# Performance work log

Measured on AMD Instinct MI355X. Metric: run time of the kernel, lower is better.

## Reference

```python
import jax, jax.numpy as jnp
import numpy as np

EPS = 1e-5

def batchnorm2d(x, gamma, beta):
    # training-mode BN over (N, T, V) per channel; x: [N, C, T, V]
    mean = jnp.mean(x, axis=(0, 2, 3), keepdims=True)
    var = jnp.var(x, axis=(0, 2, 3), keepdims=True)
    xhat = (x - mean) * jax.lax.rsqrt(var + EPS)
    return xhat * gamma[None, :, None, None] + beta[None, :, None, None]

def temporal_shift(x, theta, stride):
    # learnable per-channel temporal shift with linear interpolation, zero pad
    # x: [N, C, T, V], theta: [C]
    N, C, T, V = x.shape
    T_out = T // stride
    t = jnp.arange(T_out, dtype=theta.dtype)
    pos = t[None, :] * stride + theta[:, None]          # [C, T_out]
    i0 = jnp.floor(pos).astype(jnp.int32)
    frac = (pos - i0.astype(theta.dtype))[None, :, :, None]  # [1,C,T_out,1]
    cidx = jnp.arange(C)[:, None]                        # [C, 1]

    def gather(idx):
        valid = (idx >= 0) & (idx < T)
        g = x[:, cidx, jnp.clip(idx, 0, T - 1), :]       # [N, C, T_out, V]
        return jnp.where(valid[None, :, :, None], g, 0.0)

    return gather(i0) * (1.0 - frac) + gather(i0 + 1) * frac

def setup_inputs() -> dict:
    key = jax.random.key(0)
    k = jax.random.split(key, 6)
    N, Cin, Cout, T, V = 64, 256, 256, 64, 25
    x = jax.random.normal(k[0], (N, Cin, T, V), dtype=jnp.float32)
    # kaiming normal fan_out for 1x1 conv: std = sqrt(2 / (Cout*1*1))
    conv_w = jax.random.normal(k[1], (Cout, Cin), dtype=jnp.float32) * np.float32(np.sqrt(2.0 / Cout))
    conv_b = jnp.zeros((Cout,), dtype=jnp.float32)
    bn1_g = jnp.ones((Cin,), dtype=jnp.float32)
    bn1_b = jnp.zeros((Cin,), dtype=jnp.float32)
    bn2_g = jnp.ones((Cin,), dtype=jnp.float32)   # bn_init(bn2, 1)
    bn2_b = jnp.zeros((Cin,), dtype=jnp.float32)
    theta_in = jax.random.uniform(k[2], (Cin,), jnp.float32, -1.0, 1.0)
    theta_out = jax.random.uniform(k[3], (Cout,), jnp.float32, -1.0, 1.0)
    return {"x": x, "conv_w": conv_w, "conv_b": conv_b,
            "bn1_g": bn1_g, "bn1_b": bn1_b, "bn2_g": bn2_g, "bn2_b": bn2_b,
            "theta_in": theta_in, "theta_out": theta_out}

def reference(x, conv_w, conv_b, bn1_g, bn1_b, bn2_g, bn2_b, theta_in, theta_out):
    stride = 1
    h = batchnorm2d(x, bn1_g, bn1_b)
    h = temporal_shift(h, theta_in, 1)
    h = jnp.einsum('nctv,oc->notv', h, conv_w) + conv_b[None, :, None, None]
    h = jax.nn.relu(h)
    h = temporal_shift(h, theta_out, stride)
    h = batchnorm2d(h, bn2_g, bn2_b)
    return h
```

## Files before the change

kernel.cpp:

```cpp
#include <hip/hip_runtime.h>


#define EPSV 1e-5f
constexpr int Nn = 64, Cc = 256, Tt = 64, Vv = 25;
constexpr int TV = Tt * Vv;
constexpr int CTV = Cc * TV;
constexpr float Minv = 1.0f / (Nn * TV);

typedef short short8 __attribute__((ext_vector_type(8)));
typedef float floatx4 __attribute__((ext_vector_type(4)));

__device__ __forceinline__ unsigned short f2bf(float f) {
    unsigned int u = __builtin_bit_cast(unsigned int, f);
    u += 0x7FFFu + ((u >> 16) & 1u);
    return (unsigned short)(u >> 16);
}
__device__ __forceinline__ float bf2f(unsigned short h) {
    unsigned int u = ((unsigned int)h) << 16;
    return __builtin_bit_cast(float, u);
}
__device__ __forceinline__ float bflo(unsigned int w) {
    return __builtin_bit_cast(float, w << 16);
}
__device__ __forceinline__ float bfhi(unsigned int w) {
    return __builtin_bit_cast(float, w & 0xFFFF0000u);
}
__device__ __forceinline__ void unp8v(uint4 u, float* o) {
    o[0] = bflo(u.x); o[1] = bfhi(u.x); o[2] = bflo(u.y); o[3] = bfhi(u.y);
    o[4] = bflo(u.z); o[5] = bfhi(u.z); o[6] = bflo(u.w); o[7] = bfhi(u.w);
}
__device__ __forceinline__ void gload_lds16(const void* g, void* l) {
    __builtin_amdgcn_global_load_lds((const __attribute__((address_space(1))) void*)g,
                                     (__attribute__((address_space(3))) void*)l, 16, 0, 0);
}

__global__ __launch_bounds__(256) void k_stats_shift(const float* __restrict__ x,
                                                     const float* __restrict__ theta,
                                                     float* __restrict__ sacc,
                                                     float* __restrict__ qacc,
                                                     unsigned short* __restrict__ ht) {
    int c0 = blockIdx.x * 64;
    int E0 = blockIdx.y * 200;
    int n  = blockIdx.z;
    int tid = threadIdx.x;
    __shared__ __attribute__((aligned(16))) unsigned short xt[256][68];
    __shared__ int   pd[64];
    __shared__ float pf[64];
    if (tid < 64) {
        float th = theta[c0 + tid];
        float fd = floorf(th);
        pd[tid] = (int)fd;
        pf[tid] = th - fd;
    }
    int lo = E0 - 28; if (lo < 0) lo = 0;
    int hi = E0 + 228; if (hi > 1600) hi = 1600;
    int ldsoff = lo - (E0 - 28);
    int nf4 = (hi - lo) >> 2;
    {
        int cp = tid >> 3, li = tid & 7;
        int ca = 2 * cp;
        const float4* xr0 = (const float4*)(x + (size_t)n * CTV + (size_t)(c0 + ca) * TV + lo);
        const float4* xr1 = (const float4*)(x + (size_t)n * CTV + (size_t)(c0 + ca + 1) * TV + lo);
        float s0 = 0.f, q0 = 0.f, s1 = 0.f, q1 = 0.f;
        for (int i = li; i < nf4; i += 8) {
            float4 v0 = xr0[i], v1 = xr1[i];
            int r = ldsoff + i * 4;
#pragma unroll
            for (int k = 0; k < 4; ++k) {
                float a = ((const float*)&v0)[k];
                float b = ((const float*)&v1)[k];
                bool in = (unsigned)(r + k - 28) < 200u;
                if (in) { s0 += a; q0 += a * a; s1 += b; q1 += b * b; }
                unsigned int pk = (unsigned int)f2bf(a) | (((unsigned int)f2bf(b)) << 16);
                *(unsigned int*)&xt[r + k][ca] = pk;
            }
        }
        for (int off = 4; off; off >>= 1) {
            s0 += __shfl_down(s0, off); q0 += __shfl_down(q0, off);
            s1 += __shfl_down(s1, off); q1 += __shfl_down(q1, off);
        }
        if (li == 0) {
            atomicAdd(&sacc[c0 + ca], s0);     atomicAdd(&qacc[c0 + ca], q0);
            atomicAdd(&sacc[c0 + ca + 1], s1); atomicAdd(&qacc[c0 + ca + 1], q1);
        }
    }
    __syncthreads();
    int cseg = tid & 7, er = tid >> 3;
    int cb = cseg * 8;
    int dk[8]; float fk[8];
#pragma unroll
    for (int k = 0; k < 8; ++k) { dk[k] = pd[cb + k]; fk[k] = pf[cb + k]; }
    for (int it = 0; it < 7; ++it) {
        int tv_l = er + it * 32;
        if (tv_l >= 200) break;
        int e = E0 + tv_l;
        float A8[8], B8[8], C8[8];
        {
            const unsigned short* rA = &xt[tv_l + 3][cb];
            const unsigned short* rB = &xt[tv_l + 28][cb];
            const unsigned short* rC = &xt[tv_l + 53][cb];
            uint2 a0 = *(const uint2*)rA, a1 = *(const uint2*)(rA + 4);
            uint2 b0 = *(const uint2*)rB, b1 = *(const uint2*)(rB + 4);
            uint2 g0 = *(const uint2*)rC, g1 = *(const uint2*)(rC + 4);
            A8[0]=bflo(a0.x); A8[1]=bfhi(a0.x); A8[2]=bflo(a0.y); A8[3]=bfhi(a0.y);
            A8[4]=bflo(a1.x); A8[5]=bfhi(a1.x); A8[6]=bflo(a1.y); A8[7]=bfhi(a1.y);
            B8[0]=bflo(b0.x); B8[1]=bfhi(b0.x); B8[2]=bflo(b0.y); B8[3]=bfhi(b0.y);
            B8[4]=bflo(b1.x); B8[5]=bfhi(b1.x); B8[6]=bflo(b1.y); B8[7]=bfhi(b1.y);
            C8[0]=bflo(g0.x); C8[1]=bfhi(g0.x); C8[2]=bflo(g0.y); C8[3]=bfhi(g0.y);
            C8[4]=bflo(g1.x); C8[5]=bfhi(g1.x); C8[6]=bflo(g1.y); C8[7]=bfhi(g1.y);
        }
        unsigned int w4[4];
#pragma unroll
        for (int k = 0; k < 8; ++k) {
            int d = dk[k]; float f = fk[k];
            float x0 = (d < 0) ? A8[k] : B8[k];
            float x1 = (d < 0) ? B8[k] : C8[k];
            int e0 = e + 25 * d;
            float v0 = ((unsigned)e0 < 1600u) ? x0 : 0.f;
            float v1 = ((unsigned)(e0 + 25) < 1600u) ? x1 : 0.f;
            unsigned short hb = f2bf(v0 + f * (v1 - v0));
            if (k & 1) w4[k >> 1] |= ((unsigned int)hb) << 16;
            else       w4[k >> 1] = hb;
        }
        uint4 st = { w4[0], w4[1], w4[2], w4[3] };
        *(uint4*)(ht + (size_t)(n * 1600 + e) * 256 + c0 + cb) = st;
    }
}

__global__ __launch_bounds__(256) void k_params(const float* __restrict__ w,
                                                const float* __restrict__ bias,
                                                const float* __restrict__ sacc,
                                                const float* __restrict__ qacc,
                                                const float* __restrict__ g,
                                                const float* __restrict__ b,
                                                const float* __restrict__ theta,
                                                unsigned short* __restrict__ wb,
                                                float* __restrict__ b2all,
                                                float* __restrict__ s0v,
                                                float* __restrict__ s63v) {
    int o = blockIdx.x, c = threadIdx.x;
    float mean = sacc[c] * Minv;
    float var  = qacc[c] * Minv - mean * mean;
    float sc = g[c] * rsqrtf(var + EPSV);
    float tc = b[c] - mean * sc;
    float th = theta[c];
    float fd = floorf(th);
    int d = (int)fd;
    float f = th - fd;
    float wv = w[o * 256 + c];
    wb[o * 256 + c] = f2bf(wv * sc);
    float wtc = wv * tc;
    float r0  = (d < 0) ? wtc * (1.f - f) : 0.f;
    float r63 = (d == 0) ? wtc * f : 0.f;
    for (int off = 32; off; off >>= 1) {
        wtc += __shfl_down(wtc, off);
        r0  += __shfl_down(r0, off);
        r63 += __shfl_down(r63, off);
    }
    __shared__ float aux[3][4];
    if ((c & 63) == 0) { int wi = c >> 6; aux[0][wi] = wtc; aux[1][wi] = r0; aux[2][wi] = r63; }
    __syncthreads();
    if (c == 0) {
        b2all[o] = bias[o] + aux[0][0] + aux[0][1] + aux[0][2] + aux[0][3];
        s0v[o]  = aux[1][0] + aux[1][1] + aux[1][2] + aux[1][3];
        s63v[o] = aux[2][0] + aux[2][1] + aux[2][2] + aux[2][3];
    }
}

__global__ __launch_bounds__(256, 2) void k_gemm(const unsigned short* __restrict__ ht,
                                                 const unsigned short* __restrict__ wb,
                                                 const float* __restrict__ b2all,
                                                 const float* __restrict__ s0v,
                                                 const float* __restrict__ s63v,
                                                 unsigned short* __restrict__ y) {
    int j0 = blockIdx.x * 128;
    int tid = threadIdx.x;
    int w = tid >> 6, lane = tid & 63;
    int quad = lane >> 4, l16 = lane & 15;
    __shared__ __attribute__((aligned(16))) unsigned short smem[256 * 136];
    unsigned short* A = smem;
    unsigned short* B = smem + 256 * 32;
    floatx4 acc[4][8] = {};
    int srowA = w * 64 + (lane >> 2);
    int srowB = w * 32 + (lane >> 2);
    int skc = (lane & 3) * 8;
    const unsigned short* wp = wb + (size_t)srowA * 256 + skc;
    const unsigned short* hp = ht + (size_t)(j0 + srowB) * 256 + skc;
    for (int k0 = 0; k0 < 256; k0 += 32) {
        __syncthreads();
#pragma unroll
        for (int a = 0; a < 4; ++a)
            gload_lds16(wp + (size_t)a * 16 * 256 + k0, A + (w * 64 + a * 16) * 32);
#pragma unroll
        for (int a = 0; a < 2; ++a)
            gload_lds16(hp + (size_t)a * 16 * 256 + k0, B + (w * 32 + a * 16) * 32);
        __syncthreads();
        short8 af[4], bf[8];
#pragma unroll
        for (int m = 0; m < 4; ++m)
            af[m] = *(const short8*)&A[(w * 64 + m * 16 + l16) * 32 + quad * 8];
#pragma unroll
        for (int jt = 0; jt < 8; ++jt)
            bf[jt] = *(const short8*)&B[(jt * 16 + l16) * 32 + quad * 8];
#pragma unroll
        for (int m = 0; m < 4; ++m)
#pragma unroll
            for (int jt = 0; jt < 8; ++jt)
                acc[m][jt] = __builtin_amdgcn_mfma_f32_16x16x32_bf16(af[m], bf[jt], acc[m][jt], 0, 0, 0);
    }
    __syncthreads();
    unsigned short* Cl = smem;
#pragma unroll
    for (int m = 0; m < 4; ++m) {
        int ob = w * 64 + m * 16 + quad * 4;
#pragma unroll
        for (int r = 0; r < 4; ++r) {
            int o = ob + r;
            float bb = b2all[o], e0 = s0v[o], e63 = s63v[o];
#pragma unroll
            for (int jt = 0; jt < 8; ++jt) {
                int jj = j0 + jt * 16;
                int nn = jj / 1600;
                int tvb = jj - nn * 1600 + l16;
                float bia = bb - (tvb < 25 ? e0 : 0.f) - (tvb >= 1575 ? e63 : 0.f);
                float v = acc[m][jt][r] + bia;
                v = v > 0.f ? v : 0.f;
                Cl[o * 136 + jt * 16 + l16] = f2bf(v);
            }
        }
    }
    __syncthreads();
    int li = tid & 15, orow = tid >> 4;
#pragma unroll
    for (int pass = 0; pass < 16; ++pass) {
        int o = orow + pass * 16;
        uint4 vv = *(const uint4*)&Cl[o * 136 + li * 8];
        int j = j0 + li * 8;
        int nn = j / 1600;
        int tv = j - nn * 1600;
        *(uint4*)(y + (size_t)nn * CTV + (size_t)o * TV + tv) = vv;
    }
}

__global__ __launch_bounds__(256) void k_bn2_stats(const unsigned short* __restrict__ y,
                                                   float* __restrict__ acc7) {
    int o = blockIdx.y, ng = blockIdx.x, tid = threadIdx.x;
    float S = 0.f, Q = 0.f, P = 0.f, Y0 = 0.f, Q0 = 0.f, Y63 = 0.f, Q63 = 0.f;
    if (tid < 200) {
        int e = tid * 8;
        int eB = e + 24; if (eB > 1592) eB = 1592;
        int eC = e + 32; if (eC > 1592) eC = 1592;
        const unsigned short* base0 = y + (size_t)(ng * 8) * CTV + (size_t)o * TV;
        for (int nn = 0; nn < 8; ++nn) {
            const unsigned short* row = base0 + (size_t)nn * CTV;
            float a[8], b[8], c[8];
            unp8v(*(const uint4*)(row + e), a);
            unp8v(*(const uint4*)(row + eB), b);
            unp8v(*(const uint4*)(row + eC), c);
#pragma unroll
            for (int k = 0; k < 8; ++k) {
                float v = a[k];
                S += v; Q += v * v;
                float vn = (k < 7) ? b[k + 1] : c[0];
                if (e + k < 1575) P += v * vn;
            }
            if (e < 32) {
#pragma unroll
                for (int k = 0; k < 8; ++k)
                    if (e + k < 25) { Y0 += a[k]; Q0 += a[k] * a[k]; }
            }
            if (e >= 1568) {
#pragma unroll
                for (int k = 0; k < 8; ++k)
                    if (e + k >= 1575) { Y63 += a[k]; Q63 += a[k] * a[k]; }
            }
        }
    }
    for (int off = 32; off; off >>= 1) {
        S += __shfl_down(S, off); Q += __shfl_down(Q, off); P += __shfl_down(P, off);
        Y0 += __shfl_down(Y0, off); Q0 += __shfl_down(Q0, off);
        Y63 += __shfl_down(Y63, off); Q63 += __shfl_down(Q63, off);
    }
    if ((tid & 63) == 0) {
        atomicAdd(&acc7[o], S);           atomicAdd(&acc7[256 + o], Q);
        atomicAdd(&acc7[512 + o], P);     atomicAdd(&acc7[768 + o], Y0);
        atomicAdd(&acc7[1024 + o], Q0);   atomicAdd(&acc7[1280 + o], Y63);
        atomicAdd(&acc7[1536 + o], Q63);
    }
}

__global__ __launch_bounds__(256) void k_bn2_apply(const unsigned short* __restrict__ y,
                                                   const float* __restrict__ theta,
                                                   const float* __restrict__ acc7,
                                                   const float* __restrict__ g,
                                                   const float* __restrict__ b,
                                                   float* __restrict__ out) {
    int o = blockIdx.y, n = blockIdx.x, tid = threadIdx.x;
    float th = theta[o];
    float fd = floorf(th);
    int d = (int)fd;
    float f = th - fd;
    float S = acc7[o], Q = acc7[256 + o], P = acc7[512 + o];
    float Y0 = acc7[768 + o], Q0 = acc7[1024 + o], Y63 = acc7[1280 + o], Q63 = acc7[1536 + o];
    float omf = 1.f - f;
    float sz, qz;
    if (d < 0) { sz = S - omf * Y63; qz = omf * omf * (Q - Q63) + f * f * Q + 2.f * f * omf * P; }
    else       { sz = S - f * Y0;    qz = omf * omf * Q + f * f * (Q - Q0) + 2.f * f * omf * P; }
    float mean = sz * Minv;
    float var = qz * Minv - mean * mean;
    float sc = g[o] * rsqrtf(var + EPSV);
    float tc = b[o] - mean * sc;
    if (tid >= 200) return;
    int e = tid * 8;
    const unsigned short* row = y + (size_t)n * CTV + (size_t)o * TV;
    float a0[8], a1[8];
    if (d < 0) {
        int eA = e - 32; if (eA < 0) eA = 0;
        int eB = e - 24; if (eB < 0) eB = 0;
        float A[8], B[8], M[8];
        unp8v(*(const uint4*)(row + eA), A);
        unp8v(*(const uint4*)(row + eB), B);
        unp8v(*(const uint4*)(row + e), M);
        a0[0] = (e >= 25) ? A[7] : 0.f;
#pragma unroll
        for (int k = 1; k < 8; ++k) a0[k] = (e + k >= 25) ? B[k - 1] : 0.f;
#pragma unroll
        for (int k = 0; k < 8; ++k) a1[k] = M[k];
    } else {
        int eB = e + 24; if (eB > 1592) eB = 1592;
        int eC = e + 32; if (eC > 1592) eC = 1592;
        float M[8], B[8], C[8];
        unp8v(*(const uint4*)(row + e), M);
        unp8v(*(const uint4*)(row + eB), B);
        unp8v(*(const uint4*)(row + eC), C);
#pragma unroll
        for (int k = 0; k < 8; ++k) a0[k] = M[k];
#pragma unroll
        for (int k = 0; k < 7; ++k) a1[k] = (e + k < 1575) ? B[k + 1] : 0.f;
        a1[7] = (e + 7 < 1575) ? C[0] : 0.f;
    }
    float4 r0, r1;
#pragma unroll
    for (int k = 0; k < 4; ++k) {
        ((float*)&r0)[k] = (omf * a0[k] + f * a1[k]) * sc + tc;
        ((float*)&r1)[k] = (omf * a0[k + 4] + f * a1[k + 4]) * sc + tc;
    }
    float* op = out + (size_t)n * CTV + (size_t)o * TV + e;
    *(float4*)op = r0;
    *(float4*)(op + 4) = r1;
}

extern "C" void kernel_launch(void* const* d_in, const int* in_sizes, int n_in,
                              void* d_out, int out_size, void* d_ws, size_t ws_size,
                              hipStream_t stream) {
    const float* x      = (const float*)d_in[0];
    const float* conv_w = (const float*)d_in[1];
    const float* conv_b = (const float*)d_in[2];
    const float* bn1_g  = (const float*)d_in[3];
    const float* bn1_b  = (const float*)d_in[4];
    const float* bn2_g  = (const float*)d_in[5];
    const float* bn2_b  = (const float*)d_in[6];
    const float* th_in  = (const float*)d_in[7];
    const float* th_out = (const float*)d_in[8];
    float* out = (float*)d_out;

    char* ws = (char*)d_ws;
    unsigned short* ht = (unsigned short*)ws;
    unsigned short* yy = (unsigned short*)(ws + 52428800);
    unsigned short* wb = (unsigned short*)(ws + 104857600);
    float* sacc1 = (float*)(ws + 104988672);
    float* qacc1 = sacc1 + 256;
    float* acc7  = qacc1 + 256;
    float* b2all = acc7 + 7 * 256;
    float* s0v   = b2all + 256;
    float* s63v  = s0v + 256;

    hipMemsetAsync((void*)sacc1, 0, 9 * 256 * sizeof(float), stream);
    hipLaunchKernelGGL(k_stats_shift, dim3(4, 8, 64), dim3(256), 0, stream,
                       x, th_in, sacc1, qacc1, ht);
    hipLaunchKernelGGL(k_params, dim3(256), dim3(256), 0, stream,
                       conv_w, conv_b, sacc1, qacc1, bn1_g, bn1_b, th_in,
                       wb, b2all, s0v, s63v);
    hipLaunchKernelGGL(k_gemm, dim3(800), dim3(256), 0, stream,
                       ht, wb, b2all, s0v, s63v, yy);
    hipLaunchKernelGGL(k_bn2_stats, dim3(8, 256), dim3(256), 0, stream, yy, acc7);
    hipLaunchKernelGGL(k_bn2_apply, dim3(64, 256), dim3(256), 0, stream,
                       yy, th_out, acc7, bn2_g, bn2_b, out);
}
```

Measured before the change: 342.5 us.

## Batch loads in stats kernel, widen GEMM K-step, prefetch rows in BN2 stats

New measurement: 352.2 us. 2.8% more time.

```diff
diff --git a/kernel.cpp b/kernel.cpp
--- a/kernel.cpp
+++ b/kernel.cpp
@@ -14,10 +14,6 @@
     unsigned int u = __builtin_bit_cast(unsigned int, f);
     u += 0x7FFFu + ((u >> 16) & 1u);
     return (unsigned short)(u >> 16);
-}
-__device__ __forceinline__ float bf2f(unsigned short h) {
-    unsigned int u = ((unsigned int)h) << 16;
-    return __builtin_bit_cast(float, u);
 }
 __device__ __forceinline__ float bflo(unsigned int w) {
     return __builtin_bit_cast(float, w << 16);
@@ -60,19 +56,29 @@
         int cp = tid >> 3, li = tid & 7;
         int ca = 2 * cp;
         const float4* xr0 = (const float4*)(x + (size_t)n * CTV + (size_t)(c0 + ca) * TV + lo);
-        const float4* xr1 = (const float4*)(x + (size_t)n * CTV + (size_t)(c0 + ca + 1) * TV + lo);
+        const float4* xr1 = xr0 + (TV >> 2);
+        float4 v0[8], v1[8];
+#pragma unroll
+        for (int s = 0; s < 8; ++s) {
+            int i = li + s * 8;
+            if (i < nf4) { v0[s] = xr0[i]; v1[s] = xr1[i]; }
+        }
         float s0 = 0.f, q0 = 0.f, s1 = 0.f, q1 = 0.f;
-        for (int i = li; i < nf4; i += 8) {
-            float4 v0 = xr0[i], v1 = xr1[i];
-            int r = ldsoff + i * 4;
-#pragma unroll
-            for (int k = 0; k < 4; ++k) {
-                float a = ((const float*)&v0)[k];
-                float b = ((const float*)&v1)[k];
-                bool in = (unsigned)(r + k - 28) < 200u;
-                if (in) { s0 += a; q0 += a * a; s1 += b; q1 += b * b; }
-                unsigned int pk = (unsigned int)f2bf(a) | (((unsigned int)f2bf(b)) << 16);
-                *(unsigned int*)&xt[r + k][ca] = pk;
+#pragma unroll
+        for (int s = 0; s < 8; ++s) {
+            int i = li + s * 8;
+            if (i < nf4) {
+                int r = ldsoff + i * 4;
+#pragma unroll
+                for (int k = 0; k < 4; ++k) {
+                    float a = ((const float*)&v0[s])[k];
+                    float b = ((const float*)&v1[s])[k];
+                    if ((unsigned)(r + k - 28) < 200u) {
+                        s0 += a; q0 += a * a; s1 += b; q1 += b * b;
+                    }
+                    unsigned int pk = (unsigned int)f2bf(a) | (((unsigned int)f2bf(b)) << 16);
+                    *(unsigned int*)&xt[r + k][ca] = pk;
+                }
             }
         }
         for (int off = 4; off; off >>= 1) {
@@ -167,78 +173,89 @@
     }
 }
 
-__global__ __launch_bounds__(256, 2) void k_gemm(const unsigned short* __restrict__ ht,
-                                                 const unsigned short* __restrict__ wb,
-                                                 const float* __restrict__ b2all,
-                                                 const float* __restrict__ s0v,
-                                                 const float* __restrict__ s63v,
-                                                 unsigned short* __restrict__ y) {
+__global__ __launch_bounds__(256) void k_gemm(const unsigned short* __restrict__ ht,
+                                              const unsigned short* __restrict__ wb,
+                                              const float* __restrict__ b2all,
+                                              const float* __restrict__ s0v,
+                                              const float* __restrict__ s63v,
+                                              unsigned short* __restrict__ y) {
     int j0 = blockIdx.x * 128;
     int tid = threadIdx.x;
     int w = tid >> 6, lane = tid & 63;
     int quad = lane >> 4, l16 = lane & 15;
-    __shared__ __attribute__((aligned(16))) unsigned short smem[256 * 136];
+    __shared__ __attribute__((aligned(16))) unsigned short smem[256 * 64 + 128 * 64];
     unsigned short* A = smem;
-    unsigned short* B = smem + 256 * 32;
+    unsigned short* B = smem + 256 * 64;
     floatx4 acc[4][8] = {};
-    int srowA = w * 64 + (lane >> 2);
-    int srowB = w * 32 + (lane >> 2);
-    int skc = (lane & 3) * 8;
-    const unsigned short* wp = wb + (size_t)srowA * 256 + skc;
-    const unsigned short* hp = ht + (size_t)(j0 + srowB) * 256 + skc;
-    for (int k0 = 0; k0 < 256; k0 += 32) {
+    int srow8 = lane >> 3;
+    int skc = (lane & 7) * 8;
+    const unsigned short* wp = wb + (size_t)(w * 64 + srow8) * 256 + skc;
+    const unsigned short* hp = ht + (size_t)(j0 + w * 32 + srow8) * 256 + skc;
+    for (int k0 = 0; k0 < 256; k0 += 64) {
         __syncthreads();
 #pragma unroll
+        for (int a = 0; a < 8; ++a)
+            gload_lds16(wp + (size_t)a * 8 * 256 + k0, A + (w * 64 + a * 8) * 64);
+#pragma unroll
         for (int a = 0; a < 4; ++a)
-            gload_lds16(wp + (size_t)a * 16 * 256 + k0, A + (w * 64 + a * 16) * 32);
-#pragma unroll
-        for (int a = 0; a < 2; ++a)
-            gload_lds16(hp + (size_t)a * 16 * 256 + k0, B + (w * 32 + a * 16) * 32);
+            gload_lds16(hp + (size_t)a * 8 * 256 + k0, B + (w * 32 + a * 8) * 64);
         __syncthreads();
-        short8 af[4], bf[8];
-#pragma unroll
-        for (int m = 0; m < 4; ++m)
-            af[m] = *(const short8*)&A[(w * 64 + m * 16 + l16) * 32 + quad * 8];
-#pragma unroll
-        for (int jt = 0; jt < 8; ++jt)
-            bf[jt] = *(const short8*)&B[(jt * 16 + l16) * 32 + quad * 8];
-#pragma unroll
-        for (int m = 0; m < 4; ++m)
+#pragma unroll
+        for (int kk = 0; kk < 2; ++kk) {
+            short8 af[4], bf[8];
+#pragma unroll
+            for (int m = 0; m < 4; ++m)
+                af[m] = *(const short8*)&A[(w * 64 + m * 16 + l16) * 64 + kk * 32 + quad * 8];
 #pragma unroll
             for (int jt = 0; jt < 8; ++jt)
-                acc[m][jt] = __builtin_amdgcn_mfma_f32_16x16x32_bf16(af[m], bf[jt], acc[m][jt], 0, 0, 0);
+                bf[jt] = *(const short8*)&B[(jt * 16 + l16) * 64 + kk * 32 + quad * 8];
+#pragma unroll
+            for (int m = 0; m < 4; ++m)
+#pragma unroll
+                for (int jt = 0; jt < 8; ++jt)
+                    acc[m][jt] = __builtin_amdgcn_mfma_f32_16x16x32_bf16(af[m], bf[jt], acc[m][jt], 0, 0, 0);
+        }
     }
     __syncthreads();
     unsigned short* Cl = smem;
-#pragma unroll
-    for (int m = 0; m < 4; ++m) {
-        int ob = w * 64 + m * 16 + quad * 4;
-#pragma unroll
-        for (int r = 0; r < 4; ++r) {
-            int o = ob + r;
-            float bb = b2all[o], e0 = s0v[o], e63 = s63v[o];
-#pragma unroll
-            for (int jt = 0; jt < 8; ++jt) {
-                int jj = j0 + jt * 16;
-                int nn = jj / 1600;
-                int tvb = jj - nn * 1600 + l16;
-                float bia = bb - (tvb < 25 ? e0 : 0.f) - (tvb >= 1575 ? e63 : 0.f);
-                float v = acc[m][jt][r] + bia;
-                v = v > 0.f ? v : 0.f;
-                Cl[o * 136 + jt * 16 + l16] = f2bf(v);
-            }
-        }
-    }
-    __syncthreads();
     int li = tid & 15, orow = tid >> 4;
 #pragma unroll
-    for (int pass = 0; pass < 16; ++pass) {
-        int o = orow + pass * 16;
-        uint4 vv = *(const uint4*)&Cl[o * 136 + li * 8];
-        int j = j0 + li * 8;
-        int nn = j / 1600;
-        int tv = j - nn * 1600;
-        *(uint4*)(y + (size_t)nn * CTV + (size_t)o * TV + tv) = vv;
+    for (int p = 0; p < 2; ++p) {
+        if ((w >> 1) == p) {
+            int rowbase = (w & 1) * 64;
+#pragma unroll
+            for (int m = 0; m < 4; ++m) {
+                int ob = p * 128 + (w & 1) * 64 + m * 16 + quad * 4;
+#pragma unroll
+                for (int r = 0; r < 4; ++r) {
+                    int o = ob + r;
+                    float bb = b2all[o], e0 = s0v[o], e63 = s63v[o];
+                    int lrow = rowbase + m * 16 + quad * 4 + r;
+#pragma unroll
+                    for (int jt = 0; jt < 8; ++jt) {
+                        int jj = j0 + jt * 16;
+                        int nn = jj / 1600;
+                        int tvb = jj - nn * 1600 + l16;
+                        float bia = bb - (tvb < 25 ? e0 : 0.f) - (tvb >= 1575 ? e63 : 0.f);
+                        float v = acc[m][jt][r] + bia;
+                        v = v > 0.f ? v : 0.f;
+                        Cl[lrow * 136 + jt * 16 + l16] = f2bf(v);
+                    }
+                }
+            }
+        }
+        __syncthreads();
+#pragma unroll
+        for (int pass = 0; pass < 8; ++pass) {
+            int ol = orow + pass * 16;
+            uint4 vv = *(const uint4*)&Cl[ol * 136 + li * 8];
+            int o = p * 128 + ol;
+            int j = j0 + li * 8;
+            int nn = j / 1600;
+            int tv = j - nn * 1600;
+            *(uint4*)(y + (size_t)nn * CTV + (size_t)o * TV + tv) = vv;
+        }
+        if (p == 0) __syncthreads();
     }
 }
 
@@ -251,12 +268,19 @@
         int eB = e + 24; if (eB > 1592) eB = 1592;
         int eC = e + 32; if (eC > 1592) eC = 1592;
         const unsigned short* base0 = y + (size_t)(ng * 8) * CTV + (size_t)o * TV;
+        uint4 ua = *(const uint4*)(base0 + e);
+        uint4 ub = *(const uint4*)(base0 + eB);
+        uint4 uc = *(const uint4*)(base0 + eC);
         for (int nn = 0; nn < 8; ++nn) {
-            const unsigned short* row = base0 + (size_t)nn * CTV;
+            uint4 na, nb, nc;
+            if (nn < 7) {
+                const unsigned short* row = base0 + (size_t)(nn + 1) * CTV;
+                na = *(const uint4*)(row + e);
+                nb = *(const uint4*)(row + eB);
+                nc = *(const uint4*)(row + eC);
+            }
             float a[8], b[8], c[8];
-            unp8v(*(const uint4*)(row + e), a);
-            unp8v(*(const uint4*)(row + eB), b);
-            unp8v(*(const uint4*)(row + eC), c);
+            unp8v(ua, a); unp8v(ub, b); unp8v(uc, c);
 #pragma unroll
             for (int k = 0; k < 8; ++k) {
                 float v = a[k];
@@ -274,6 +298,7 @@
                 for (int k = 0; k < 8; ++k)
                     if (e + k >= 1575) { Y63 += a[k]; Q63 += a[k] * a[k]; }
             }
+            ua = na; ub = nb; uc = nc;
         }
     }
     for (int off = 32; off; off >>= 1) {
```
